# Performance work log

Measured on AMD Instinct MI355X. Metric: run time of the kernel, lower is better.

## Reference

```python
import jax, jax.numpy as jnp
import numpy as np

B, C, H, W = 8, 384, 32, 32
NH, DK, DV = 8, 48, 48
CFF = 4 * C
L = H * W
NBIAS = (2 * H - 1) * (2 * W - 1)
LN_EPS = 1e-5


def _relative_indices(height, width):
    # rel_idx[q, k] = (gy_k - gy_q + H) * W + (gx_k - gx_q + W), matching the torch loop
    gy, gx = np.meshgrid(np.arange(height), np.arange(width), indexing='ij')
    gy = gy.ravel(); gx = gx.ravel()
    rel = (gy[None, :] - gy[:, None] + height) * width + (gx[None, :] - gx[:, None] + width)
    return jnp.asarray(rel, dtype=jnp.int64)


def setup_inputs() -> dict:
    key = jax.random.key(0)
    ks = jax.random.split(key, 10)
    s = 0.02  # small init scale
    return {
        'x': jax.random.normal(ks[0], (B, C, H, W), dtype=jnp.float32),
        'gamma': jnp.ones((C,), jnp.float32),
        'beta': jnp.zeros((C,), jnp.float32),
        'Wq': jax.random.normal(ks[1], (NH * DK, C), jnp.float32) * s,
        'Wk': jax.random.normal(ks[2], (NH * DK, C), jnp.float32) * s,
        'Wv': jax.random.normal(ks[3], (NH * DV, C), jnp.float32) * s,
        'Wo': jax.random.normal(ks[4], (C, NH * DV), jnp.float32) * s,
        'bo': jnp.zeros((C,), jnp.float32),
        'rel_bias': jax.random.normal(ks[5], (NH, NBIAS), jnp.float32),
        'fc1_w': jax.random.normal(ks[6], (CFF, C), jnp.float32) * s,
        'fc1_b': jnp.zeros((CFF,), jnp.float32),
        'fc2_w': jax.random.normal(ks[7], (C, CFF), jnp.float32) * s,
        'fc2_b': jnp.zeros((C,), jnp.float32),
        'rel_idx': _relative_indices(H, W),
    }


def reference(x, gamma, beta, Wq, Wk, Wv, Wo, bo, rel_bias,
              fc1_w, fc1_b, fc2_w, fc2_b, rel_idx):
    b, c, h_sp, w_sp = x.shape
    l = h_sp * w_sp
    nh = rel_bias.shape[0]
    dk = Wq.shape[0] // nh
    dv = Wv.shape[0] // nh

    # LayerNorm over channel dim (NHWC), then flatten to tokens [b, l, c]
    t = jnp.transpose(x, (0, 2, 3, 1))
    mu = jnp.mean(t, axis=-1, keepdims=True)
    var = jnp.mean(jnp.square(t - mu), axis=-1, keepdims=True)
    t = (t - mu) / jnp.sqrt(var + LN_EPS) * gamma + beta
    tok = t.reshape(b, l, c)

    q = (tok @ Wq.T).reshape(b, l, nh, dk)
    k = (tok @ Wk.T).reshape(b, l, nh, dk)
    v = (tok @ Wv.T).reshape(b, l, nh, dv)

    # gathered relative position bias: [nh, l, l]
    bias = rel_bias[:, rel_idx]
    # note: original applies NO 1/sqrt(d_k) scaling
    scores = jnp.einsum('blhd,bmhd->bhlm', q, k) + bias[None]
    attn = jax.nn.softmax(scores, axis=-1)
    out = jnp.einsum('bhlm,bmhd->blhd', attn, v).reshape(b, l, nh * dv)
    out = out @ Wo.T + bo  # [b, l, c]
    out = jnp.transpose(out, (0, 2, 1)).reshape(b, c, h_sp, w_sp)

    y = x + out  # attention residual (x_stem = x, no downsampling)

    # FFN: 1x1 convs == per-pixel linear over channels; exact (erf) gelu as torch default
    u = jnp.einsum('bchw,oc->bohw', y, fc1_w) + fc1_b[None, :, None, None]
    u = jax.nn.gelu(u, approximate=False)
    u = jnp.einsum('bchw,oc->bohw', u, fc2_w) + fc2_b[None, :, None, None]
    return y + u
```

## Files before the change

### kernel.cpp

```cpp
#include <hip/hip_runtime.h>
#include <math.h>

#define SL 1024
#define CH 384
#define NHEAD 8
#define DH 48
#define NBIAS 3969
#define NTOK 8192
#define BATCH 8
#define CFF 1536
#define LN_EPS 1e-5f
#define QKVLD 1152
#define HMS 3145728
#define LOG2E 1.4426950408889634f

#define WQKV_OFF 0
#define WO_OFF   442368
#define F1_OFF   589824
#define F2_OFF   1179648
#define WTOT     1769472

typedef float floatx4 __attribute__((ext_vector_type(4)));
typedef short bf16x8 __attribute__((ext_vector_type(8)));

__device__ __forceinline__ unsigned f2bf_u(float f) {
  unsigned u = __float_as_uint(f);
  return (u + 0x7fffu + ((u >> 16) & 1u)) >> 16;
}
__device__ __forceinline__ unsigned pack2(float a, float b) {
  return f2bf_u(a) | (f2bf_u(b) << 16);
}
__device__ __forceinline__ unsigned cvtpk(float lo, float hi) {
  unsigned r;
  asm("v_cvt_pk_bf16_f32 %0, %1, %2" : "=v"(r) : "v"(lo), "v"(hi));
  return r;
}

__device__ __forceinline__ void gload_lds16(const void* g, void* l) {
  __builtin_amdgcn_global_load_lds(
      (const __attribute__((address_space(1))) void*)g,
      (__attribute__((address_space(3))) void*)l, 16, 0, 0);
}

__global__ void k_w2bf(const float* __restrict__ Wq, const float* __restrict__ Wk,
                       const float* __restrict__ Wv, const float* __restrict__ Wo,
                       const float* __restrict__ f1, const float* __restrict__ f2,
                       short* __restrict__ dst) {
  size_t i = ((size_t)blockIdx.x * 256 + threadIdx.x) * 8;
  if (i >= WTOT) return;
  const float* s;
  size_t base;
  if (i < 147456)        { s = Wq; base = 0; }
  else if (i < 294912)   { s = Wk; base = 147456; }
  else if (i < WO_OFF)   { s = Wv; base = 294912; }
  else if (i < F1_OFF)   { s = Wo; base = WO_OFF; }
  else if (i < F2_OFF)   { s = f1; base = F1_OFF; }
  else                   { s = f2; base = F2_OFF; }
  const float4* p = (const float4*)(s + (i - base));
  float4 a = p[0], b = p[1];
  uint4 o;
  o.x = pack2(a.x, a.y); o.y = pack2(a.z, a.w);
  o.z = pack2(b.x, b.y); o.w = pack2(b.z, b.w);
  *(uint4*)(dst + i) = o;
}

__global__ __launch_bounds__(256) void k_ln_fused(
    const float* __restrict__ x, const float* __restrict__ gamma,
    const float* __restrict__ beta, short* __restrict__ tok) {
  __shared__ float sx[32][385];
  int b = blockIdx.y, l0 = blockIdx.x * 32;
  int tid = threadIdx.x;
  const float* xb = x + (size_t)b * CH * SL;
  int cr = tid >> 3, ls = (tid & 7) * 4;
#pragma unroll
  for (int c0 = 0; c0 < CH; c0 += 32) {
    int c = c0 + cr;
    float4 v = *(const float4*)(xb + (size_t)c * SL + l0 + ls);
    sx[ls + 0][c] = v.x; sx[ls + 1][c] = v.y;
    sx[ls + 2][c] = v.z; sx[ls + 3][c] = v.w;
  }
  __syncthreads();
  int tl = tid >> 3, p = tid & 7;
  float vals[48];
  float s = 0.f, q = 0.f;
#pragma unroll
  for (int i = 0; i < 48; i++) {
    float v = sx[tl][p * 48 + i];
    vals[i] = v; s += v; q += v * v;
  }
  s += __shfl_xor(s, 1, 64); q += __shfl_xor(q, 1, 64);
  s += __shfl_xor(s, 2, 64); q += __shfl_xor(q, 2, 64);
  s += __shfl_xor(s, 4, 64); q += __shfl_xor(q, 4, 64);
  float mu = s * (1.0f / CH);
  float rstd = rsqrtf(q * (1.0f / CH) - mu * mu + LN_EPS);
  short* orow = tok + (size_t)(b * SL + l0 + tl) * CH + p * 48;
#pragma unroll
  for (int i = 0; i < 48; i += 2) {
    float a = (vals[i] - mu) * rstd * gamma[p * 48 + i] + beta[p * 48 + i];
    float c = (vals[i + 1] - mu) * rstd * gamma[p * 48 + i + 1] + beta[p * 48 + i + 1];
    *(unsigned*)(orow + i) = pack2(a, c);
  }
}

template <int BM, bool GELU, bool HAS_BIAS, int RES_MODE, int OUT_MODE>
__global__ __launch_bounds__(256) void k_gemm_mfma(
    const short* __restrict__ A, const short* __restrict__ W,
    const float* __restrict__ bias, const float* __restrict__ res,
    float* __restrict__ Cf, short* __restrict__ Cb, float* __restrict__ Ct,
    short* __restrict__ Chm, int N, int K) {
  constexpr int MI = BM / 32;
  constexpr int ASI = BM * 2 / 64;
  __shared__ short As[2][BM * 64];
  __shared__ short Bs[2][128 * 64];
  int tid = threadIdx.x;
  int wid = tid >> 6, lane = tid & 63;
  int lanelo = lane & 15, quad = lane >> 4;
  int wm = wid & 1, wn = wid >> 1;

  int nbx = (int)gridDim.x;
  int lin = (int)blockIdx.y * nbx + (int)blockIdx.x;
  int chunk = (nbx * (int)gridDim.y) >> 3;
  int wk = (lin & 7) * chunk + (lin >> 3);
  int m0 = (wk / nbx) * BM, n0 = (wk % nbx) * 128;

  const short* Aga[ASI];
  short* Ala[ASI];
#pragma unroll
  for (int s = 0; s < ASI; s++) {
    int p = wid * (BM * 2) + s * 64 + lane;
    int row = p >> 3, ch = (p & 7) ^ (row & 7);
    Aga[s] = A + (size_t)(m0 + row) * K + ch * 8;
    Ala[s] = &As[0][0] + (wid * (BM * 2) + s * 64) * 8;
  }
  const short* Bga[4];
  short* Bla[4];
#pragma unroll
  for (int s = 0; s < 4; s++) {
    int p = wid * 256 + s * 64 + lane;
    int row = p >> 3, ch = (p & 7) ^ (row & 7);
    Bga[s] = W + (size_t)(n0 + row) * K + ch * 8;
    Bla[s] = &Bs[0][0] + (wid * 256 + s * 64) * 8;
  }

  floatx4 acc[MI][4];
#pragma unroll
  for (int i = 0; i < MI; i++)
#pragma unroll
    for (int j = 0; j < 4; j++) acc[i][j] = {0.f, 0.f, 0.f, 0.f};

  int x8 = lanelo & 7;
  int ca0 = (quad ^ x8) * 8;
  int ca1 = ((quad + 4) ^ x8) * 8;

#pragma unroll
  for (int s = 0; s < ASI; s++) gload_lds16(Aga[s], Ala[s]);
#pragma unroll
  for (int s = 0; s < 4; s++) gload_lds16(Bga[s], Bla[s]);
  __syncthreads();

  int cur = 0;
  for (int k0 = 0; k0 < K; k0 += 64) {
    int nxt = cur ^ 1;
    if (k0 + 64 < K) {
#pragma unroll
      for (int s = 0; s < ASI; s++)
        gload_lds16(Aga[s] + k0 + 64, Ala[s] + nxt * (BM * 64));
#pragma unroll
      for (int s = 0; s < 4; s++)
        gload_lds16(Bga[s] + k0 + 64, Bla[s] + nxt * (128 * 64));
    }
#pragma unroll
    for (int h = 0; h < 2; h++) {
      int co = h ? ca1 : ca0;
      bf16x8 af[MI], bq[4];
#pragma unroll
      for (int i = 0; i < MI; i++)
        af[i] = *(const bf16x8*)&As[cur][(wm * (BM / 2) + i * 16 + lanelo) * 64 + co];
#pragma unroll
      for (int j = 0; j < 4; j++)
        bq[j] = *(const bf16x8*)&Bs[cur][(wn * 64 + j * 16 + lanelo) * 64 + co];
#pragma unroll
      for (int i = 0; i < MI; i++)
#pragma unroll
        for (int j = 0; j < 4; j++)
          acc[i][j] = __builtin_amdgcn_mfma_f32_16x16x32_bf16(af[i], bq[j], acc[i][j], 0, 0, 0);
    }
    __syncthreads();
    cur = nxt;
  }

  int colb = n0 + wn * 64 + lanelo;
  float bvv[4];
#pragma unroll
  for (int j = 0; j < 4; j++) bvv[j] = HAS_BIAS ? bias[colb + j * 16] : 0.0f;
#pragma unroll
  for (int i = 0; i < MI; i++) {
    int r = m0 + wm * (BM / 2) + i * 16 + quad * 4;
    int bb = r >> 10, ll = r & 1023;
#pragma unroll
    for (int j = 0; j < 4; j++) {
      int c = colb + j * 16;
      float4 rv = {0.f, 0.f, 0.f, 0.f};
      if (RES_MODE == 2) rv = *(const float4*)(res + ((size_t)bb * CH + c) * SL + ll);
      float vv[4];
#pragma unroll
      for (int reg = 0; reg < 4; reg++) {
        float v = acc[i][j][reg] + bvv[j];
        if (RES_MODE == 1) v += res[(size_t)(r + reg) * N + c];
        if (RES_MODE == 2) v += (&rv.x)[reg];
        if (GELU) {
          float t = v * fmaf(v * v, 0.0356774081f, 0.7978845608f);
          float e = __builtin_amdgcn_exp2f(t * -2.8853900817779268f);
          v = v * __builtin_amdgcn_rcpf(e + 1.0f);
        }
        vv[reg] = v;
      }
      if (OUT_MODE & 1) {
#pragma unroll
        for (int reg = 0; reg < 4; reg++) Cf[(size_t)(r + reg) * N + c] = vv[reg];
      }
      if (OUT_MODE & 2) {
#pragma unroll
        for (int reg = 0; reg < 4; reg++) Cb[(size_t)(r + reg) * N + c] = (short)f2bf_u(vv[reg]);
      }
      if (OUT_MODE & 4) {
        float4 ov = {vv[0], vv[1], vv[2], vv[3]};
        *(float4*)(Ct + ((size_t)bb * CH + c) * SL + ll) = ov;
      }
      if (OUT_MODE & 8) {
        int part = c / 384;
        int rem = c - part * 384;
        int hh = rem / 48, dd = rem - hh * 48;
        short* dst = Chm + (size_t)part * HMS +
                     ((size_t)(bb * NHEAD + hh) * SL + ll) * 48 + dd;
#pragma unroll
        for (int reg = 0; reg < 4; reg++) dst[reg * 48] = (short)f2bf_u(vv[reg]);
      }
    }
  }
}

__global__ __launch_bounds__(256) void k_attn_mfma(
    const short* __restrict__ qh, const short* __restrict__ kh,
    const short* __restrict__ vh, const float* __restrict__ rel_bias,
    short* __restrict__ ao) {
  __shared__ short QP[128 * 72];
  __shared__ short Ks[2][64 * 72];
  __shared__ short Vts[2][48 * 72];
  float* Bb = (float*)QP;

  int lin = ((int)blockIdx.z * 8 + (int)blockIdx.y) * 8 + (int)blockIdx.x;
  int wk = (lin & 7) * 64 + (lin >> 3);
  int b = wk >> 6, h = (wk >> 3) & 7;
  int l0 = (wk & 7) * 128;
  int tid = threadIdx.x;
  int wid = tid >> 6, lane = tid & 63;
  int lanelo = lane & 15, quad = lane >> 4;
  size_t hb = ((size_t)b * NHEAD + h) * SL;
  size_t bSL = (size_t)b * SL;
  const short* kbase = kh + hb * 48;
  const short* vbase = vh + hb * 48;

  {
    const short* qsrc = qh + (hb + l0) * 48;
#pragma unroll
    for (int s = 0; s < 3; s++) {
      int g = tid + 256 * s;
      int row = g / 6, pos = g - row * 6;
      *(uint4*)&QP[row * 72 + pos * 8] = *(const uint4*)(qsrc + g * 8);
    }
  }
  for (int z = tid; z < 128 * 8; z += 256) {
    int r = z >> 3, u = z & 7;
    ((unsigned*)&QP[r * 72 + 48])[u] = 0u;
    if (r < 64) {
      ((unsigned*)&Ks[0][r * 72 + 48])[u] = 0u;
      ((unsigned*)&Ks[1][r * 72 + 48])[u] = 0u;
    }
  }
  __syncthreads();

  bf16x8 aq[2][2];
#pragma unroll
  for (int qi = 0; qi < 2; qi++) {
    aq[qi][0] = *(const bf16x8*)&QP[(wid * 32 + qi * 16 + lanelo) * 72 + quad * 8];
    aq[qi][1] = *(const bf16x8*)&QP[(wid * 32 + qi * 16 + lanelo) * 72 + 32 + quad * 8];
  }
  __syncthreads();

  int kg = 2 * tid;
  int krow = kg / 6, kpos = kg - krow * 6;
  int vmp = tid & 31, vdg = tid >> 5;
  int kk = 2 * vmp;
  int vcol = (kk & 3) + ((kk >> 2) & 3) * 8 + ((kk >> 4) & 1) * 4 + (kk >> 5) * 32;
  unsigned sel_e = 0x05040100u, sel_o = 0x07060302u;

  {
    const float* bsrc = rel_bias + h * NBIAS + (929 - l0);
    for (int j = tid; j < 1152; j += 256) Bb[j] = bsrc[j] * LOG2E;
  }
  if (tid < 192) {
    const short* ksrc = kbase + kg * 8;
    uint4 k0 = *(const uint4*)(ksrc);
    uint4 k1 = *(const uint4*)(ksrc + 8);
    const short* vs = vbase + (size_t)kk * 48 + vdg * 8;
    uint4 va = *(const uint4*)vs;
    uint4 vb = *(const uint4*)(vs + 48);
    *(uint4*)&Ks[0][krow * 72 + kpos * 8] = k0;
    *(uint4*)&Ks[0][krow * 72 + (kpos + 1) * 8] = k1;
#pragma unroll
    for (int j = 0; j < 4; j++) {
      unsigned wa = ((const unsigned*)&va)[j], wb = ((const unsigned*)&vb)[j];
      unsigned pe, po;
      asm("v_perm_b32 %0, %1, %2, %3" : "=v"(pe) : "v"(wb), "v"(wa), "v"(sel_e));
      asm("v_perm_b32 %0, %1, %2, %3" : "=v"(po) : "v"(wb), "v"(wa), "v"(sel_o));
      *(unsigned*)&Vts[0][(vdg * 8 + 2 * j + 0) * 72 + vcol] = pe;
      *(unsigned*)&Vts[0][(vdg * 8 + 2 * j + 1) * 72 + vcol] = po;
    }
  }
  __syncthreads();

  floatx4 O[3][2];
#pragma unroll
  for (int dt = 0; dt < 3; dt++)
#pragma unroll
    for (int qi = 0; qi < 2; qi++) O[dt][qi] = {0.f, 0.f, 0.f, 0.f};
  float lsum[2] = {0.f, 0.f};
  int boff[2];
#pragma unroll
  for (int qi = 0; qi < 2; qi++)
    boff[qi] = 127 + quad * 4 - (wid * 32 + qi * 16 + lanelo);

  int cur = 0;
  for (int mt = 0; mt < SL; mt += 64) {
    bool last = (mt + 64 >= SL);
    uint4 k0n, k1n, van, vbn;
    if (tid < 192 && !last) {
      int mtn = mt + 64;
      const short* ksrc = kbase + (size_t)mtn * 48 + kg * 8;
      k0n = *(const uint4*)(ksrc);
      k1n = *(const uint4*)(ksrc + 8);
      const short* vs = vbase + (size_t)(mtn + kk) * 48 + vdg * 8;
      van = *(const uint4*)vs;
      vbn = *(const uint4*)(vs + 48);
    }

    bf16x8 kb[4][2];
#pragma unroll
    for (int nt = 0; nt < 4; nt++) {
      kb[nt][0] = *(const bf16x8*)&Ks[cur][(nt * 16 + lanelo) * 72 + quad * 8];
      kb[nt][1] = *(const bf16x8*)&Ks[cur][(nt * 16 + lanelo) * 72 + 32 + quad * 8];
    }
    bf16x8 vf[3][2];
#pragma unroll
    for (int dt = 0; dt < 3; dt++) {
      vf[dt][0] = *(const bf16x8*)&Vts[cur][(dt * 16 + lanelo) * 72 + quad * 8];
      vf[dt][1] = *(const bf16x8*)&Vts[cur][(dt * 16 + lanelo) * 72 + 32 + quad * 8];
    }

#pragma unroll
    for (int qi = 0; qi < 2; qi++) {
      floatx4 sc[4];
#pragma unroll
      for (int nt = 0; nt < 4; nt++) {
        floatx4 a = {0.f, 0.f, 0.f, 0.f};
        a = __builtin_amdgcn_mfma_f32_16x16x32_bf16(kb[nt][0], aq[qi][0], a, 0, 0, 0);
        a = __builtin_amdgcn_mfma_f32_16x16x32_bf16(kb[nt][1], aq[qi][1], a, 0, 0, 0);
        sc[nt] = a;
      }
      union U8 { unsigned u[4]; bf16x8 v; };
      U8 pb0, pb1;
#pragma unroll
      for (int nt = 0; nt < 4; nt++) {
        int bidx = boff[qi] + mt + nt * 16;
        float e0 = __builtin_amdgcn_exp2f(fmaf(sc[nt][0], LOG2E, Bb[bidx + 0]));
        float e1 = __builtin_amdgcn_exp2f(fmaf(sc[nt][1], LOG2E, Bb[bidx + 1]));
        float e2 = __builtin_amdgcn_exp2f(fmaf(sc[nt][2], LOG2E, Bb[bidx + 2]));
        float e3 = __builtin_amdgcn_exp2f(fmaf(sc[nt][3], LOG2E, Bb[bidx + 3]));
        lsum[qi] += (e0 + e1) + (e2 + e3);
        unsigned p01 = cvtpk(e0, e1), p23 = cvtpk(e2, e3);
        if (nt == 0) { pb0.u[0] = p01; pb0.u[1] = p23; }
        else if (nt == 1) { pb0.u[2] = p01; pb0.u[3] = p23; }
        else if (nt == 2) { pb1.u[0] = p01; pb1.u[1] = p23; }
        else { pb1.u[2] = p01; pb1.u[3] = p23; }
      }
#pragma unroll
      for (int dt = 0; dt < 3; dt++) {
        O[dt][qi] = __builtin_amdgcn_mfma_f32_16x16x32_bf16(vf[dt][0], pb0.v, O[dt][qi], 0, 0, 0);
        O[dt][qi] = __builtin_amdgcn_mfma_f32_16x16x32_bf16(vf[dt][1], pb1.v, O[dt][qi], 0, 0, 0);
      }
    }

    if (tid < 192 && !last) {
      int nxt = cur ^ 1;
      *(uint4*)&Ks[nxt][krow * 72 + kpos * 8] = k0n;
      *(uint4*)&Ks[nxt][krow * 72 + (kpos + 1) * 8] = k1n;
#pragma unroll
      for (int j = 0; j < 4; j++) {
        unsigned wa = ((const unsigned*)&van)[j], wb = ((const unsigned*)&vbn)[j];
        unsigned pe, po;
        asm("v_perm_b32 %0, %1, %2, %3" : "=v"(pe) : "v"(wb), "v"(wa), "v"(sel_e));
        asm("v_perm_b32 %0, %1, %2, %3" : "=v"(po) : "v"(wb), "v"(wa), "v"(sel_o));
        *(unsigned*)&Vts[nxt][(vdg * 8 + 2 * j + 0) * 72 + vcol] = pe;
        *(unsigned*)&Vts[nxt][(vdg * 8 + 2 * j + 1) * 72 + vcol] = po;
      }
    }
    __syncthreads();
    cur ^= 1;
  }

  __syncthreads();
  float inv[2];
#pragma unroll
  for (int qi = 0; qi < 2; qi++) {
    float s = lsum[qi];
    s += __shfl_xor(s, 16, 64);
    s += __shfl_xor(s, 32, 64);
    inv[qi] = __builtin_amdgcn_rcpf(s);
  }
#pragma unroll
  for (int dt = 0; dt < 3; dt++)
#pragma unroll
    for (int qi = 0; qi < 2; qi++) {
      unsigned w0 = cvtpk(O[dt][qi][0] * inv[qi], O[dt][qi][1] * inv[qi]);
      unsigned w1 = cvtpk(O[dt][qi][2] * inv[qi], O[dt][qi][3] * inv[qi]);
      uint2 wv = {w0, w1};
      *(uint2*)&QP[(wid * 32 + qi * 16 + lanelo) * 72 + dt * 16 + quad * 4] = wv;
    }
  __asm__ volatile("s_waitcnt lgkmcnt(0)" ::: "memory");
#pragma unroll
  for (int s = 0; s < 3; s++) {
    int g = lane + 64 * s;
    int qloc = g / 6, pos = g - qloc * 6;
    uint4 val = *(const uint4*)&QP[(wid * 32 + qloc) * 72 + pos * 8];
    *(uint4*)(ao + (bSL + (size_t)(l0 + wid * 32 + qloc)) * CH + h * DH + pos * 8) = val;
  }
}

extern "C" void kernel_launch(void* const* d_in, const int* in_sizes, int n_in,
                              void* d_out, int out_size, void* d_ws, size_t ws_size,
                              hipStream_t stream) {
  const float* x = (const float*)d_in[0];
  const float* gamma = (const float*)d_in[1];
  const float* beta = (const float*)d_in[2];
  const float* Wq = (const float*)d_in[3];
  const float* Wk = (const float*)d_in[4];
  const float* Wv = (const float*)d_in[5];
  const float* Wo = (const float*)d_in[6];
  const float* bo = (const float*)d_in[7];
  const float* rel_bias = (const float*)d_in[8];
  const float* fc1_w = (const float*)d_in[9];
  const float* fc1_b = (const float*)d_in[10];
  const float* fc2_w = (const float*)d_in[11];
  const float* fc2_b = (const float*)d_in[12];
  float* out = (float*)d_out;

  const size_t TOKCH = (size_t)NTOK * CH;
  float* ws_f = (float*)d_ws;
  float* yb = ws_f;
  short* wbf    = (short*)(yb + TOKCH);
  short* tok_bf = wbf + WTOT;
  short* hm     = tok_bf + TOKCH;
  short* ao_bf  = hm + 3 * (size_t)HMS;
  short* yb_bf  = ao_bf + TOKCH;
  short* h1_bf  = yb_bf + TOKCH;

  k_w2bf<<<WTOT / 8 / 256, 256, 0, stream>>>(Wq, Wk, Wv, Wo, fc1_w, fc2_w, wbf);
  k_ln_fused<<<dim3(SL / 32, BATCH), 256, 0, stream>>>(x, gamma, beta, tok_bf);

  k_gemm_mfma<64, false, false, 0, 8>
      <<<dim3(QKVLD / 128, NTOK / 64), 256, 0, stream>>>(
          tok_bf, wbf + WQKV_OFF, nullptr, nullptr, nullptr, nullptr, nullptr,
          hm, QKVLD, CH);

  k_attn_mfma<<<dim3(SL / 128, NHEAD, BATCH), 256, 0, stream>>>(
      hm, hm + HMS, hm + 2 * (size_t)HMS, rel_bias, ao_bf);

  k_gemm_mfma<64, false, true, 2, 3>
      <<<dim3(CH / 128, NTOK / 64), 256, 0, stream>>>(
          ao_bf, wbf + WO_OFF, bo, x, yb, yb_bf, nullptr, nullptr, CH, CH);

  k_gemm_mfma<64, true, true, 0, 2>
      <<<dim3(CFF / 128, NTOK / 64), 256, 0, stream>>>(
          yb_bf, wbf + F1_OFF, fc1_b, nullptr, nullptr, h1_bf, nullptr, nullptr,
          CFF, CH);

  k_gemm_mfma<64, false, true, 1, 4>
      <<<dim3(CH / 128, NTOK / 64), 256, 0, stream>>>(
          h1_bf, wbf + F2_OFF, fc2_b, yb, nullptr, nullptr, out, nullptr, CH, CFF);
}
```

Before: 199.3 us.

## Prefetch two K-tiles ahead in MFMA GEMM and enlarge M tile for QKV/FC1

Restructures the GEMM main loop so global-to-LDS loads run two tiles ahead. It uses explicit vmcnt waits and raw s_barrier in place of __syncthreads, so loads overlap more of the MFMA work. The QKV and FC1 GEMMs also switch from a 64-row to a 128-row M tile, halving the grid and increasing reuse of each B tile. The risks are fewer blocks for latency hiding and higher register/LDS use with BM=128. Correctness now depends on the hand-written waitcnt counts being right.

After: 200.4 us. No clear change (+0.6%).

```diff
diff --git a/kernel.cpp b/kernel.cpp
--- a/kernel.cpp
+++ b/kernel.cpp
@@ -110,6 +110,7 @@
     short* __restrict__ Chm, int N, int K) {
   constexpr int MI = BM / 32;
   constexpr int ASI = BM * 2 / 64;
+  constexpr int NLD = ASI + 4;
   __shared__ short As[2][BM * 64];
   __shared__ short Bs[2][128 * 64];
   int tid = threadIdx.x;
@@ -152,41 +153,54 @@
   int ca0 = (quad ^ x8) * 8;
   int ca1 = ((quad + 4) ^ x8) * 8;
 
+  int ntile = K >> 6;
 #pragma unroll
   for (int s = 0; s < ASI; s++) gload_lds16(Aga[s], Ala[s]);
 #pragma unroll
   for (int s = 0; s < 4; s++) gload_lds16(Bga[s], Bla[s]);
-  __syncthreads();
-
-  int cur = 0;
-  for (int k0 = 0; k0 < K; k0 += 64) {
-    int nxt = cur ^ 1;
-    if (k0 + 64 < K) {
-#pragma unroll
-      for (int s = 0; s < ASI; s++)
-        gload_lds16(Aga[s] + k0 + 64, Ala[s] + nxt * (BM * 64));
-#pragma unroll
-      for (int s = 0; s < 4; s++)
-        gload_lds16(Bga[s] + k0 + 64, Bla[s] + nxt * (128 * 64));
-    }
+#pragma unroll
+  for (int s = 0; s < ASI; s++) gload_lds16(Aga[s] + 64, Ala[s] + BM * 64);
+#pragma unroll
+  for (int s = 0; s < 4; s++) gload_lds16(Bga[s] + 64, Bla[s] + 128 * 64);
+  asm volatile("s_waitcnt vmcnt(%0)" :: "n"(NLD) : "memory");
+  __builtin_amdgcn_sched_barrier(0);
+  __builtin_amdgcn_s_barrier();
+
+  for (int t = 0; t < ntile; t++) {
+    int cb = t & 1;
+    const short* Asb = &As[cb][0];
+    const short* Bsb = &Bs[cb][0];
 #pragma unroll
     for (int h = 0; h < 2; h++) {
       int co = h ? ca1 : ca0;
       bf16x8 af[MI], bq[4];
 #pragma unroll
       for (int i = 0; i < MI; i++)
-        af[i] = *(const bf16x8*)&As[cur][(wm * (BM / 2) + i * 16 + lanelo) * 64 + co];
+        af[i] = *(const bf16x8*)&Asb[(wm * (BM / 2) + i * 16 + lanelo) * 64 + co];
 #pragma unroll
       for (int j = 0; j < 4; j++)
-        bq[j] = *(const bf16x8*)&Bs[cur][(wn * 64 + j * 16 + lanelo) * 64 + co];
+        bq[j] = *(const bf16x8*)&Bsb[(wn * 64 + j * 16 + lanelo) * 64 + co];
 #pragma unroll
       for (int i = 0; i < MI; i++)
 #pragma unroll
         for (int j = 0; j < 4; j++)
           acc[i][j] = __builtin_amdgcn_mfma_f32_16x16x32_bf16(af[i], bq[j], acc[i][j], 0, 0, 0);
     }
-    __syncthreads();
-    cur = nxt;
+    __builtin_amdgcn_s_barrier();
+    if (t + 2 < ntile) {
+      int ko = (t + 2) * 64;
+#pragma unroll
+      for (int s = 0; s < ASI; s++)
+        gload_lds16(Aga[s] + ko, Ala[s] + cb * (BM * 64));
+#pragma unroll
+      for (int s = 0; s < 4; s++)
+        gload_lds16(Bga[s] + ko, Bla[s] + cb * (128 * 64));
+      asm volatile("s_waitcnt vmcnt(%0)" :: "n"(NLD) : "memory");
+    } else {
+      asm volatile("s_waitcnt vmcnt(0)" ::: "memory");
+    }
+    __builtin_amdgcn_sched_barrier(0);
+    __builtin_amdgcn_s_barrier();
   }
 
   int colb = n0 + wn * 64 + lanelo;
@@ -468,8 +482,8 @@
   k_w2bf<<<WTOT / 8 / 256, 256, 0, stream>>>(Wq, Wk, Wv, Wo, fc1_w, fc2_w, wbf);
   k_ln_fused<<<dim3(SL / 32, BATCH), 256, 0, stream>>>(x, gamma, beta, tok_bf);
 
-  k_gemm_mfma<64, false, false, 0, 8>
-      <<<dim3(QKVLD / 128, NTOK / 64), 256, 0, stream>>>(
+  k_gemm_mfma<128, false, false, 0, 8>
+      <<<dim3(QKVLD / 128, NTOK / 128), 256, 0, stream>>>(
           tok_bf, wbf + WQKV_OFF, nullptr, nullptr, nullptr, nullptr, nullptr,
           hm, QKVLD, CH);
 
@@ -480,8 +494,8 @@
       <<<dim3(CH / 128, NTOK / 64), 256, 0, stream>>>(
           ao_bf, wbf + WO_OFF, bo, x, yb, yb_bf, nullptr, nullptr, CH, CH);
 
-  k_gemm_mfma<64, true, true, 0, 2>
-      <<<dim3(CFF / 128, NTOK / 64), 256, 0, stream>>>(
+  k_gemm_mfma<128, true, true, 0, 2>
+      <<<dim3(CFF / 128, NTOK / 128), 256, 0, stream>>>(
           yb_bf, wbf + F1_OFF, fc1_b, nullptr, nullptr, h1_bf, nullptr, nullptr,
           CFF, CH);
 
```
